# Performance work log

Hardware: AMD Instinct MI355X
Metric: run time of the kernel (lower is better)

Reference implementation:

```python
import jax, jax.numpy as jnp
import numpy as np

EPS = 1e-16  # cell's self.epsilon


def setup_inputs() -> dict:
    key = jax.random.key(0)
    M, B, Q, L = 2, 64, 512, 512  # num_models, batch, max_num_states, seq_len
    k1, k2, k3 = jax.random.split(key, 3)
    # row-stochastic transition matrices per model (transitioner's dense A)
    A = jax.nn.softmax(jax.random.normal(k1, (M, Q, Q), jnp.float32), axis=-1)
    # initial state distribution per model
    init_dist = jax.nn.softmax(jax.random.normal(k2, (M, Q), jnp.float32), axis=-1)
    # precomputed emission probabilities per step (output of self.emission_probs)
    emission_probs = jax.random.uniform(k3, (L, M, B, Q), jnp.float32)
    return {"emission_probs": emission_probs, "A": A, "init_dist": init_dist}


def reference(emission_probs, A, init_dist):
    """Full scaled forward algorithm = RNN over HmmCell.call (parallel_factor=1).

    emission_probs: (L, M, B, Q)  A: (M, Q, Q)  init_dist: (M, Q)
    Returns per-sequence log-likelihood of shape (M, B).
    """
    def one_step(R, E, old_ll):
        # HmmCell.call body: clamp, multiply, renormalize, accumulate loglik
        E = jnp.maximum(E, EPS)
        R = jnp.maximum(R, EPS)
        sf = E * R                                  # (M, B, Q)
        S = jnp.sum(sf, axis=-1, keepdims=True)     # (M, B, 1)
        ll = old_ll + jnp.log(S[..., 0])            # (M, B)
        return sf / S, ll

    # init step (init=True): R is the initial distribution itself
    E0 = emission_probs[0]
    R0 = jnp.broadcast_to(init_dist[:, None, :], E0.shape)
    sf0, ll0 = one_step(R0, E0, jnp.zeros(E0.shape[:2], E0.dtype))

    def scan_step(carry, E):
        sf, ll = carry
        R = jnp.einsum('mbq,mqk->mbk', sf, A)       # transitioner application
        sf, ll = one_step(R, E, ll)
        return (sf, ll), None

    (sf, ll), _ = jax.lax.scan(scan_step, (sf0, ll0), emission_probs[1:])
    return ll
```

## Files before the change

### kernel.cpp

```cpp
#include <hip/hip_runtime.h>


typedef _Float16 h2 __attribute__((ext_vector_type(2)));
typedef _Float16 h8 __attribute__((ext_vector_type(8)));

constexpr int Q = 512;
constexpr int L = 512;
constexpr int M = 2;
constexpr int B = 64;
constexpr int NTH = 1024;
constexpr int CHUNKS = 32;
constexpr int REG_CH = 24;
constexpr int LDS_CH = 8;
constexpr float EPS = 1e-16f;

constexpr int LDSA_BYTES = LDS_CH * NTH * 16;
constexpr int LDSU_OFF   = LDSA_BYTES;
constexpr int RED_OFF    = LDSU_OFF + 1024;
constexpr int RED2_OFF   = RED_OFF + 8 * Q * 4;
constexpr int SMEM_BYTES = RED2_OFF + 16;

__device__ __forceinline__ float fdot2(h2 a, h2 b, float c) {
#if __has_builtin(__builtin_amdgcn_fdot2)
    return __builtin_amdgcn_fdot2(a, b, c, false);
#else
    return fmaf((float)a.x, (float)b.x, fmaf((float)a.y, (float)b.y, c));
#endif
}

__global__ __launch_bounds__(256) void pack_A(const float* __restrict__ A,
                                              uint4* __restrict__ wsA) {
    int idx = blockIdx.x * 256 + threadIdx.x;
    int t = idx & (NTH - 1);
    int c = (idx >> 10) & (CHUNKS - 1);
    int m = idx >> 15;
    int qg = t >> 7, ct = t & 127;
    int q0 = qg * 64 + 2 * c;
    const float* a0 = A + ((size_t)m * Q + q0) * Q + 4 * ct;
    float4 r0 = *(const float4*)a0;
    float4 r1 = *(const float4*)(a0 + Q);
    union { h2 w[4]; uint4 v; } cv;
    cv.w[0].x = (_Float16)r0.x; cv.w[0].y = (_Float16)r1.x;
    cv.w[1].x = (_Float16)r0.y; cv.w[1].y = (_Float16)r1.y;
    cv.w[2].x = (_Float16)r0.z; cv.w[2].y = (_Float16)r1.z;
    cv.w[3].x = (_Float16)r0.w; cv.w[3].y = (_Float16)r1.w;
    wsA[idx] = cv.v;
}

__global__ __launch_bounds__(NTH) void hmm_fwd(
    const float* __restrict__ emis,
    const uint4* __restrict__ wsA,
    const float* __restrict__ initd,
    float* __restrict__ out)
{
    extern __shared__ char smem[];
    uint4* ldsA = (uint4*)smem;
    h2*    ldsU = (h2*)(smem + LDSU_OFF);
    float* red  = (float*)(smem + RED_OFF);
    float* red2 = (float*)(smem + RED2_OFF);

    const int t   = threadIdx.x;
    const int bid = blockIdx.x;
    const int m   = bid >> 6;
    const int qg  = t >> 7;
    const int ct  = t & 127;

    const uint4* wa = wsA + (size_t)m * CHUNKS * NTH + t;
    h8 areg[REG_CH];
    #pragma unroll
    for (int c = 0; c < REG_CH; ++c)
        areg[c] = *(const h8*)(wa + (size_t)c * NTH);
    #pragma unroll
    for (int s = 0; s < LDS_CH; ++s)
        ldsA[s * NTH + t] = wa[(size_t)(REG_CH + s) * NTH];

    const float* E = emis + (size_t)bid * Q;
    const size_t stepStride = (size_t)M * B * Q;

    if (t < 256) {
        float2 ip = *(const float2*)(initd + m * Q + 2 * t);
        float2 ep = *(const float2*)(E + 2 * t);
        float u0 = fmaxf(ep.x, EPS) * fmaxf(ip.x, EPS);
        float u1 = fmaxf(ep.y, EPS) * fmaxf(ip.y, EPS);
        h2 w; w.x = (_Float16)u0; w.y = (_Float16)u1;
        ldsU[t] = w;
        float s = u0 + u1;
        #pragma unroll
        for (int off = 32; off >= 1; off >>= 1) s += __shfl_xor(s, off, 64);
        if ((t & 63) == 0) red2[t >> 6] = s;
    }
    __syncthreads();

    float4 r2 = *(const float4*)red2;
    float S = (r2.x + r2.y) + (r2.z + r2.w);
    float invS = 1.0f / S;
    float ll = __logf(S);

    for (int step = 1; step < L; ++step) {
        float2 ep; ep.x = 0.f; ep.y = 0.f;
        if (t < 256)
            ep = *(const float2*)(E + (size_t)step * stepStride + 2 * t);

        float a0 = 0.f, a1 = 0.f, a2 = 0.f, a3 = 0.f;
        const h8* uq8 = (const h8*)(ldsU + qg * 32);
        #pragma unroll
        for (int i = 0; i < 8; ++i) {
            h8 uw = uq8[i];
            h2 up[4] = {uw.lo.lo, uw.lo.hi, uw.hi.lo, uw.hi.hi};
            #pragma unroll
            for (int p = 0; p < 4; ++p) {
                const int c = i * 4 + p;
                h8 a;
                if (c < REG_CH) a = areg[c];
                else            a = *(const h8*)(ldsA + (c - REG_CH) * NTH + t);
                a0 = fdot2(a.lo.lo, up[p], a0);
                a1 = fdot2(a.lo.hi, up[p], a1);
                a2 = fdot2(a.hi.lo, up[p], a2);
                a3 = fdot2(a.hi.hi, up[p], a3);
            }
        }
        float4 rv; rv.x = a0; rv.y = a1; rv.z = a2; rv.w = a3;
        *(float4*)(red + qg * Q + 4 * ct) = rv;
        __syncthreads();

        if (t < 256) {
            float r0 = 0.f, r1 = 0.f;
            #pragma unroll
            for (int g = 0; g < 8; ++g) {
                float2 rp = *(const float2*)(red + g * Q + 2 * t);
                r0 += rp.x; r1 += rp.y;
            }
            float u0 = fmaxf(ep.x, EPS) * fmaxf(r0 * invS, EPS);
            float u1 = fmaxf(ep.y, EPS) * fmaxf(r1 * invS, EPS);
            h2 w; w.x = (_Float16)u0; w.y = (_Float16)u1;
            ldsU[t] = w;
            float s = u0 + u1;
            #pragma unroll
            for (int off = 32; off >= 1; off >>= 1) s += __shfl_xor(s, off, 64);
            if ((t & 63) == 0) red2[t >> 6] = s;
        }
        __syncthreads();

        r2 = *(const float4*)red2;
        S = (r2.x + r2.y) + (r2.z + r2.w);
        invS = 1.0f / S;
        ll += __logf(S);
    }

    if (t == 0) out[bid] = ll;
}

__global__ __launch_bounds__(512) void hmm_forward_fb(
    const float* __restrict__ emis, const float* __restrict__ Aall,
    const float* __restrict__ initd, float* __restrict__ out)
{
    const int bid = blockIdx.x;
    const int m = bid / B;
    const int k = threadIdx.x;
    const int lane = k & 63, wid = k >> 6;
    const float* Am = Aall + (size_t)m * Q * Q;
    const float* E = emis + (size_t)bid * Q;
    const size_t stepStride = (size_t)M * B * Q;
    __shared__ float u_lds[Q];
    __shared__ float redf[8];
    float e = fmaxf(E[k], EPS);
    float r = fmaxf(initd[m * Q + k], EPS);
    float uval = e * r;
    float ll = 0.0f, invS = 1.0f;
    for (int t = 1; t <= L; ++t) {
        float ws = uval;
        #pragma unroll
        for (int off = 32; off >= 1; off >>= 1) ws += __shfl_xor(ws, off, 64);
        __syncthreads();
        u_lds[k] = uval;
        if (lane == 0) redf[wid] = ws;
        __syncthreads();
        float S = 0.0f;
        #pragma unroll
        for (int w = 0; w < 8; ++w) S += redf[w];
        ll += __logf(S);
        invS = 1.0f / S;
        if (t == L) break;
        float acc = 0.0f;
        #pragma unroll 8
        for (int q = 0; q < Q; ++q)
            acc = fmaf(u_lds[q], Am[q * Q + k], acc);
        float rr = fmaxf(acc * invS, EPS);
        float ee = fmaxf(E[(size_t)t * stepStride + k], EPS);
        uval = ee * rr;
    }
    if (k == 0) out[bid] = ll;
}

extern "C" void kernel_launch(void* const* d_in, const int* in_sizes, int n_in,
                              void* d_out, int out_size, void* d_ws, size_t ws_size,
                              hipStream_t stream) {
    const float* emis  = (const float*)d_in[0];
    const float* A     = (const float*)d_in[1];
    const float* initd = (const float*)d_in[2];
    float* out = (float*)d_out;

    const size_t wsNeeded = (size_t)M * CHUNKS * NTH * 16;
    if (ws_size < wsNeeded) {
        hipLaunchKernelGGL(hmm_forward_fb, dim3(M * B), dim3(512), 0, stream,
                           emis, A, initd, out);
        return;
    }

    uint4* wsA = (uint4*)d_ws;
    (void)hipFuncSetAttribute((const void*)hmm_fwd,
                              hipFuncAttributeMaxDynamicSharedMemorySize,
                              SMEM_BYTES);
    hipLaunchKernelGGL(pack_A, dim3(M * CHUNKS * NTH / 256), dim3(256), 0,
                       stream, A, wsA);
    hipLaunchKernelGGL(hmm_fwd, dim3(M * B), dim3(NTH), SMEM_BYTES, stream,
                       emis, wsA, initd, out);
}
```

Measured before the change: 976.8 us.

## Keep all of A in registers and defer per-step normalization via double-buffered sums

All 32 chunks of the packed fp16 transition matrix now stay in registers, so the per-step LDS reads of the last eight chunks go away. The normalization sum is double-buffered, and the scale and log-likelihood update are folded into the next step's epilogue. The epilogue now uses 512 threads, one state each, pairing values with a lane shuffle. Holding 128 VGPRs of A per thread in a 1024-thread block risks register spills to scratch.

```diff
diff --git a/kernel.cpp b/kernel.cpp
--- a/kernel.cpp
+++ b/kernel.cpp
@@ -10,15 +10,7 @@
 constexpr int B = 64;
 constexpr int NTH = 1024;
 constexpr int CHUNKS = 32;
-constexpr int REG_CH = 24;
-constexpr int LDS_CH = 8;
 constexpr float EPS = 1e-16f;
-
-constexpr int LDSA_BYTES = LDS_CH * NTH * 16;
-constexpr int LDSU_OFF   = LDSA_BYTES;
-constexpr int RED_OFF    = LDSU_OFF + 1024;
-constexpr int RED2_OFF   = RED_OFF + 8 * Q * 4;
-constexpr int SMEM_BYTES = RED2_OFF + 16;
 
 __device__ __forceinline__ float fdot2(h2 a, h2 b, float c) {
 #if __has_builtin(__builtin_amdgcn_fdot2)
@@ -53,101 +45,103 @@
     const float* __restrict__ initd,
     float* __restrict__ out)
 {
-    extern __shared__ char smem[];
-    uint4* ldsA = (uint4*)smem;
-    h2*    ldsU = (h2*)(smem + LDSU_OFF);
-    float* red  = (float*)(smem + RED_OFF);
-    float* red2 = (float*)(smem + RED2_OFF);
+    __shared__ h2    ldsU[Q / 2];
+    __shared__ float red[8 * Q];
+    __shared__ float red2[2][8];
 
     const int t   = threadIdx.x;
     const int bid = blockIdx.x;
     const int m   = bid >> 6;
     const int qg  = t >> 7;
-    const int ct  = t & 127;
 
     const uint4* wa = wsA + (size_t)m * CHUNKS * NTH + t;
-    h8 areg[REG_CH];
+    h8 areg[CHUNKS];
     #pragma unroll
-    for (int c = 0; c < REG_CH; ++c)
+    for (int c = 0; c < CHUNKS; ++c)
         areg[c] = *(const h8*)(wa + (size_t)c * NTH);
-    #pragma unroll
-    for (int s = 0; s < LDS_CH; ++s)
-        ldsA[s * NTH + t] = wa[(size_t)(REG_CH + s) * NTH];
 
     const float* E = emis + (size_t)bid * Q;
     const size_t stepStride = (size_t)M * B * Q;
 
-    if (t < 256) {
-        float2 ip = *(const float2*)(initd + m * Q + 2 * t);
-        float2 ep = *(const float2*)(E + 2 * t);
-        float u0 = fmaxf(ep.x, EPS) * fmaxf(ip.x, EPS);
-        float u1 = fmaxf(ep.y, EPS) * fmaxf(ip.y, EPS);
-        h2 w; w.x = (_Float16)u0; w.y = (_Float16)u1;
-        ldsU[t] = w;
-        float s = u0 + u1;
+    float ll = 0.0f;
+
+    if (t < Q) {
+        float u = fmaxf(E[t], EPS) * fmaxf(initd[m * Q + t], EPS);
+        float uy = __shfl_xor(u, 1, 64);
+        if (!(t & 1)) { h2 w; w.x = (_Float16)u; w.y = (_Float16)uy; ldsU[t >> 1] = w; }
+        float s = u;
         #pragma unroll
         for (int off = 32; off >= 1; off >>= 1) s += __shfl_xor(s, off, 64);
-        if ((t & 63) == 0) red2[t >> 6] = s;
+        if ((t & 63) == 0) red2[0][t >> 6] = s;
     }
     __syncthreads();
 
-    float4 r2 = *(const float4*)red2;
-    float S = (r2.x + r2.y) + (r2.z + r2.w);
-    float invS = 1.0f / S;
-    float ll = __logf(S);
+    const float* Ep = E + stepStride + t;
 
     for (int step = 1; step < L; ++step) {
-        float2 ep; ep.x = 0.f; ep.y = 0.f;
-        if (t < 256)
-            ep = *(const float2*)(E + (size_t)step * stepStride + 2 * t);
+        const int pp = (step + 1) & 1;
+        const int cp = step & 1;
+
+        float ep = 0.0f;
+        if (t < Q) ep = *Ep;
+        Ep += stepStride;
 
         float a0 = 0.f, a1 = 0.f, a2 = 0.f, a3 = 0.f;
         const h8* uq8 = (const h8*)(ldsU + qg * 32);
         #pragma unroll
         for (int i = 0; i < 8; ++i) {
             h8 uw = uq8[i];
-            h2 up[4] = {uw.lo.lo, uw.lo.hi, uw.hi.lo, uw.hi.hi};
-            #pragma unroll
-            for (int p = 0; p < 4; ++p) {
-                const int c = i * 4 + p;
-                h8 a;
-                if (c < REG_CH) a = areg[c];
-                else            a = *(const h8*)(ldsA + (c - REG_CH) * NTH + t);
-                a0 = fdot2(a.lo.lo, up[p], a0);
-                a1 = fdot2(a.lo.hi, up[p], a1);
-                a2 = fdot2(a.hi.lo, up[p], a2);
-                a3 = fdot2(a.hi.hi, up[p], a3);
-            }
+            h2 up0 = uw.lo.lo, up1 = uw.lo.hi, up2 = uw.hi.lo, up3 = uw.hi.hi;
+            a0 = fdot2(areg[4 * i + 0].lo.lo, up0, a0);
+            a1 = fdot2(areg[4 * i + 0].lo.hi, up0, a1);
+            a2 = fdot2(areg[4 * i + 0].hi.lo, up0, a2);
+            a3 = fdot2(areg[4 * i + 0].hi.hi, up0, a3);
+            a0 = fdot2(areg[4 * i + 1].lo.lo, up1, a0);
+            a1 = fdot2(areg[4 * i + 1].lo.hi, up1, a1);
+            a2 = fdot2(areg[4 * i + 1].hi.lo, up1, a2);
+            a3 = fdot2(areg[4 * i + 1].hi.hi, up1, a3);
+            a0 = fdot2(areg[4 * i + 2].lo.lo, up2, a0);
+            a1 = fdot2(areg[4 * i + 2].lo.hi, up2, a1);
+            a2 = fdot2(areg[4 * i + 2].hi.lo, up2, a2);
+            a3 = fdot2(areg[4 * i + 2].hi.hi, up2, a3);
+            a0 = fdot2(areg[4 * i + 3].lo.lo, up3, a0);
+            a1 = fdot2(areg[4 * i + 3].lo.hi, up3, a1);
+            a2 = fdot2(areg[4 * i + 3].hi.lo, up3, a2);
+            a3 = fdot2(areg[4 * i + 3].hi.hi, up3, a3);
         }
         float4 rv; rv.x = a0; rv.y = a1; rv.z = a2; rv.w = a3;
-        *(float4*)(red + qg * Q + 4 * ct) = rv;
-        __syncthreads();
-
-        if (t < 256) {
-            float r0 = 0.f, r1 = 0.f;
+        *(float4*)(&red[qg * Q + 4 * (t & 127)]) = rv;
+        __syncthreads();
+
+        if (t < Q) {
+            float4 rA = *(const float4*)&red2[pp][0];
+            float4 rB = *(const float4*)&red2[pp][4];
+            float acc = 0.f;
             #pragma unroll
-            for (int g = 0; g < 8; ++g) {
-                float2 rp = *(const float2*)(red + g * Q + 2 * t);
-                r0 += rp.x; r1 += rp.y;
-            }
-            float u0 = fmaxf(ep.x, EPS) * fmaxf(r0 * invS, EPS);
-            float u1 = fmaxf(ep.y, EPS) * fmaxf(r1 * invS, EPS);
-            h2 w; w.x = (_Float16)u0; w.y = (_Float16)u1;
-            ldsU[t] = w;
-            float s = u0 + u1;
+            for (int g = 0; g < 8; ++g) acc += red[g * Q + t];
+            float Sv = ((rA.x + rA.y) + (rA.z + rA.w)) +
+                       ((rB.x + rB.y) + (rB.z + rB.w));
+            float inv = 1.0f / Sv;
+            ll += __logf(Sv);
+            float r = fmaxf(acc * inv, EPS);
+            float e = fmaxf(ep, EPS);
+            float u = e * r;
+            float uy = __shfl_xor(u, 1, 64);
+            if (!(t & 1)) { h2 w; w.x = (_Float16)u; w.y = (_Float16)uy; ldsU[t >> 1] = w; }
+            float s = u;
             #pragma unroll
             for (int off = 32; off >= 1; off >>= 1) s += __shfl_xor(s, off, 64);
-            if ((t & 63) == 0) red2[t >> 6] = s;
+            if ((t & 63) == 0) red2[cp][t >> 6] = s;
         }
         __syncthreads();
-
-        r2 = *(const float4*)red2;
-        S = (r2.x + r2.y) + (r2.z + r2.w);
-        invS = 1.0f / S;
-        ll += __logf(S);
-    }
-
-    if (t == 0) out[bid] = ll;
+    }
+
+    if (t == 0) {
+        const float* r2 = red2[(L - 1) & 1];
+        float Sv = ((r2[0] + r2[1]) + (r2[2] + r2[3])) +
+                   ((r2[4] + r2[5]) + (r2[6] + r2[7]));
+        out[bid] = ll + __logf(Sv);
+    }
 }
 
 __global__ __launch_bounds__(512) void hmm_forward_fb(
@@ -208,11 +202,8 @@
     }
 
     uint4* wsA = (uint4*)d_ws;
-    (void)hipFuncSetAttribute((const void*)hmm_fwd,
-                              hipFuncAttributeMaxDynamicSharedMemorySize,
-                              SMEM_BYTES);
     hipLaunchKernelGGL(pack_A, dim3(M * CHUNKS * NTH / 256), dim3(256), 0,
                        stream, A, wsA);
-    hipLaunchKernelGGL(hmm_fwd, dim3(M * B), dim3(NTH), SMEM_BYTES, stream,
+    hipLaunchKernelGGL(hmm_fwd, dim3(M * B), dim3(NTH), 0, stream,
                        emis, wsA, initd, out);
 }
```

Result: slower. 2.076 ms (+112.6%).
